# Kernel tuning notes

Measured on AMD Instinct MI355X. Metric: run time of the kernel, lower is better.

## Reference

```python
import jax, jax.numpy as jnp
import numpy as np

N, E, EL = 100000, 1600000, 200000
DIN, DH, DOUT = 128, 128, 64


def _glorot(k, fi, fo):
    return jax.random.normal(k, (fi, fo), jnp.float32) * jax.lax.rsqrt(jnp.float32(fi))


def setup_inputs() -> dict:
    key = jax.random.key(0)
    ks = jax.random.split(key, 8)
    x = jax.random.normal(ks[0], (N, DIN), jnp.float32)
    edge_index = jax.random.randint(ks[1], (2, E), 0, N)
    edge_label_index = jax.random.randint(ks[2], (2, EL), 0, N)
    return {
        "x": x,
        "W1": _glorot(ks[3], DIN, DH), "b1": jnp.zeros((DH,), jnp.float32),
        "W2": _glorot(ks[4], DH, DH), "b2": jnp.zeros((DH,), jnp.float32),
        "W3": _glorot(ks[5], DH, DOUT), "b3": jnp.zeros((DOUT,), jnp.float32),
        "edge_index": edge_index,
        "edge_label_index": edge_label_index,
    }


def gcn_conv(x, W, b, src, dst, norm, n):
    # PyG GCNConv: h = x @ W; out[dst] += norm * h[src]; out += b
    h = x @ W
    msg = h[src] * norm[:, None]                       # [E+N, d]
    out = jax.ops.segment_sum(msg, dst, num_segments=n)
    return out + b


def reference(x, W1, b1, W2, b2, W3, b3, edge_index, edge_label_index):
    n = x.shape[0]
    loop = jnp.arange(n, dtype=edge_index.dtype)
    src = jnp.concatenate([edge_index[0], loop])       # self-loops appended
    dst = jnp.concatenate([edge_index[1], loop])
    # symmetric normalization: deg from dst (col), norm = d^-1/2[src] * d^-1/2[dst]
    deg = jax.ops.segment_sum(jnp.ones(dst.shape[0], x.dtype), dst, num_segments=n)
    dis = jnp.where(deg > 0, jax.lax.rsqrt(jnp.maximum(deg, 1.0)), 0.0)
    norm = dis[src] * dis[dst]

    z = jax.nn.relu(gcn_conv(x, W1, b1, src, dst, norm, n))
    z = jax.nn.relu(gcn_conv(z, W2, b2, src, dst, norm, n))
    z = gcn_conv(z, W3, b3, src, dst, norm, n)

    # decode
    hidden = z[edge_label_index[0]] * z[edge_label_index[1]]   # [EL, DOUT]
    logits = hidden.sum(axis=-1)                               # [EL]
    nrm = jnp.maximum(jnp.linalg.norm(hidden, axis=1, keepdims=True), 1e-12)
    hidden_n = hidden / nrm                                    # F.normalize(dim=1)
    return (hidden_n, logits)
```

## Files before the change

kernel.cpp:

```cpp
#include <hip/hip_runtime.h>
#include <hip/hip_bf16.h>

#define DIN 128
#define DH  128
#define DOUT 64

#define BSHIFT 9
#define BNODES 512
#define BCAP   12288
#define CHUNK  2048

typedef __attribute__((ext_vector_type(8))) short short8;
typedef __attribute__((ext_vector_type(4))) float f32x4;

static __device__ __forceinline__ unsigned short f2bf(float f) {
    unsigned int u = __float_as_uint(f);
    u += 0x7FFFu + ((u >> 16) & 1u);
    return (unsigned short)(u >> 16);
}
static __device__ __forceinline__ float bflo(unsigned int p) {
    return __uint_as_float(p << 16);
}
static __device__ __forceinline__ float bfhi(unsigned int p) {
    return __uint_as_float(p & 0xFFFF0000u);
}

__global__ __launch_bounds__(256) void prep_w_kernel(const float* __restrict__ W1,
                                                     const float* __restrict__ W2,
                                                     const float* __restrict__ W3,
                                                     unsigned short* __restrict__ Wt1,
                                                     unsigned short* __restrict__ Wt2,
                                                     unsigned short* __restrict__ Wt3,
                                                     int* __restrict__ gcur) {
    int i = blockIdx.x * 256 + threadIdx.x;
    if (blockIdx.x == 0) gcur[threadIdx.x] = 0;
    if (i < 128 * 128) {
        int n = i >> 7, k = i & 127;
        Wt1[n * 128 + k] = f2bf(W1[k * 128 + n]);
        Wt2[n * 128 + k] = f2bf(W2[k * 128 + n]);
        if (n < 64) Wt3[n * 128 + k] = f2bf(W3[k * 64 + n]);
    }
}

__global__ __launch_bounds__(256) void bin_scatter_kernel(const int* __restrict__ ei, int E,
                                                          int* __restrict__ gcur,
                                                          int* __restrict__ pairs) {
    __shared__ int hist[256];
    __shared__ int base[256];
    int t = threadIdx.x;
    hist[t] = 0;
    __syncthreads();
    int e0 = blockIdx.x * CHUNK;
    int srcs[8], dsts[8], rk[8];
    #pragma unroll
    for (int j = 0; j < 8; j++) {
        int e = e0 + j * 256 + t;
        if (e < E) {
            srcs[j] = ei[e];
            dsts[j] = ei[E + e];
            rk[j] = atomicAdd(&hist[dsts[j] >> BSHIFT], 1);
        } else {
            rk[j] = -1;
        }
    }
    __syncthreads();
    base[t] = (hist[t] > 0) ? atomicAdd(&gcur[t], hist[t]) : 0;
    __syncthreads();
    #pragma unroll
    for (int j = 0; j < 8; j++) {
        if (rk[j] >= 0) {
            int b = dsts[j] >> BSHIFT;
            int dl = dsts[j] & (BNODES - 1);
            pairs[(size_t)b * BCAP + base[b] + rk[j]] = (dl << 17) | srcs[j];
        }
    }
}

__global__ __launch_bounds__(256) void scan_buckets_kernel(const int* __restrict__ gcur,
                                                           int* __restrict__ bucket_base,
                                                           int nbuck, int n) {
    __shared__ int s[256];
    int t = threadIdx.x;
    int own = 0;
    if (t < nbuck) {
        int lo = t << BSHIFT;
        int cnt = n - lo;
        if (cnt > BNODES) cnt = BNODES;
        if (cnt < 0) cnt = 0;
        own = gcur[t] + cnt;
    }
    s[t] = own;
    __syncthreads();
    for (int off = 1; off < 256; off <<= 1) {
        int v = (t >= off) ? s[t - off] : 0;
        __syncthreads();
        s[t] += v;
        __syncthreads();
    }
    if (t < nbuck) bucket_base[t] = s[t] - own;
}

__global__ __launch_bounds__(1024) void bucket_build_kernel(const int* __restrict__ pairs,
                                                            const int* __restrict__ gcur,
                                                            const int* __restrict__ bucket_base,
                                                            int* __restrict__ row_start,
                                                            float* __restrict__ dis,
                                                            int* __restrict__ csr_src, int n) {
    __shared__ int cnt[BNODES];
    __shared__ int snode[BNODES];
    int t = threadIdx.x, b = blockIdx.x;
    if (t < BNODES) cnt[t] = 0;
    __syncthreads();
    int m = gcur[b];
    const int* p = pairs + (size_t)b * BCAP;
    for (int i = t; i < m; i += 1024) {
        atomicAdd(&cnt[p[i] >> 17], 1);
    }
    __syncthreads();
    if (t < BNODES) {
        int node = (b << BSHIFT) + t;
        snode[t] = (node < n) ? cnt[t] + 1 : 0;
    }
    __syncthreads();
    for (int off = 1; off < BNODES; off <<= 1) {
        int v = (t < BNODES && t >= off) ? snode[t - off] : 0;
        __syncthreads();
        if (t < BNODES) snode[t] += v;
        __syncthreads();
    }
    int bbase = bucket_base[b];
    if (t < BNODES) {
        int node = (b << BSHIFT) + t;
        if (node < n) {
            int deg = cnt[t] + 1;
            int ex = bbase + snode[t] - deg;
            row_start[node] = ex;
            dis[node] = rsqrtf((float)deg);
            csr_src[ex] = node;
            cnt[t] = ex + 1;
            if (node == n - 1) row_start[n] = ex + deg;
        }
    }
    __syncthreads();
    for (int i = t; i < m; i += 1024) {
        int pk = p[i];
        int pos = atomicAdd(&cnt[pk >> 17], 1);
        csr_src[pos] = pk & 0x1FFFF;
    }
}

template <int NOUT, bool AFP32>
__global__ __launch_bounds__(256) void gemm_bf16_kernel(const void* __restrict__ Av,
                                                        const unsigned short* __restrict__ Wt,
                                                        const float* __restrict__ dis,
                                                        unsigned short* __restrict__ H, int M) {
    int wave = (blockIdx.x * 256 + threadIdx.x) >> 6;
    int lane = threadIdx.x & 63;
    int m0 = wave << 4;
    if (m0 >= M) return;
    int m = lane & 15, q = lane >> 4;
    constexpr int NT = NOUT / 16;
    f32x4 acc[NT];
    #pragma unroll
    for (int t = 0; t < NT; t++) acc[t] = (f32x4){0.f, 0.f, 0.f, 0.f};
    const short8* Arow = (const short8*)((const unsigned short*)Av + (size_t)(m0 + m) * 128);
    const float*  Arow32 = (const float*)Av + (size_t)(m0 + m) * 128;
    #pragma unroll
    for (int kk = 0; kk < 4; kk++) {
        short8 a;
        if (AFP32) {
            float4 u = *(const float4*)(Arow32 + kk * 32 + q * 8);
            float4 v = *(const float4*)(Arow32 + kk * 32 + q * 8 + 4);
            a[0] = (short)f2bf(u.x); a[1] = (short)f2bf(u.y);
            a[2] = (short)f2bf(u.z); a[3] = (short)f2bf(u.w);
            a[4] = (short)f2bf(v.x); a[5] = (short)f2bf(v.y);
            a[6] = (short)f2bf(v.z); a[7] = (short)f2bf(v.w);
        } else {
            a = Arow[kk * 4 + q];
        }
        #pragma unroll
        for (int t = 0; t < NT; t++) {
            const short8* Bp = (const short8*)(Wt + (size_t)(t * 16 + m) * 128);
            short8 b = Bp[kk * 4 + q];
            acc[t] = __builtin_amdgcn_mfma_f32_16x16x32_bf16(a, b, acc[t], 0, 0, 0);
        }
    }
    float ds[4];
    #pragma unroll
    for (int r = 0; r < 4; r++) ds[r] = dis[m0 + q * 4 + r];
    #pragma unroll
    for (int t = 0; t < NT; t++)
        #pragma unroll
        for (int r = 0; r < 4; r++)
            H[(size_t)(m0 + q * 4 + r) * NOUT + t * 16 + m] = f2bf(acc[t][r] * ds[r]);
}

template <int NOUT>
__global__ __launch_bounds__(256) void agg_gemm_kernel(const unsigned short* __restrict__ H,
                                                       const int* __restrict__ row_start,
                                                       const int* __restrict__ csr_src,
                                                       const float* __restrict__ dis,
                                                       const float* __restrict__ bias,
                                                       const unsigned short* __restrict__ Wt,
                                                       unsigned short* __restrict__ Hout,
                                                       int n) {
    __shared__ unsigned short X[16][128];
    int t = threadIdx.x;
    int g = t >> 4, gl = t & 15;
    int row = blockIdx.x * 16 + g;
    int c = gl * 8;
    float acc[8];
    #pragma unroll
    for (int i = 0; i < 8; i++) acc[i] = 0.f;
    if (row < n) {
        int p0 = row_start[row], p1 = row_start[row + 1];
        int p = p0;
        for (; p + 8 <= p1; p += 8) {
            int e[8];
            #pragma unroll
            for (int u = 0; u < 8; u++) e[u] = csr_src[p + u];
            uint4 h[8];
            #pragma unroll
            for (int u = 0; u < 8; u++) h[u] = *(const uint4*)(H + (size_t)e[u] * 128 + c);
            #pragma unroll
            for (int u = 0; u < 8; u++) {
                acc[0] += bflo(h[u].x); acc[1] += bfhi(h[u].x);
                acc[2] += bflo(h[u].y); acc[3] += bfhi(h[u].y);
                acc[4] += bflo(h[u].z); acc[5] += bfhi(h[u].z);
                acc[6] += bflo(h[u].w); acc[7] += bfhi(h[u].w);
            }
        }
        for (; p + 4 <= p1; p += 4) {
            int e0 = csr_src[p],     e1 = csr_src[p + 1];
            int e2 = csr_src[p + 2], e3 = csr_src[p + 3];
            uint4 h0 = *(const uint4*)(H + (size_t)e0 * 128 + c);
            uint4 h1 = *(const uint4*)(H + (size_t)e1 * 128 + c);
            uint4 h2 = *(const uint4*)(H + (size_t)e2 * 128 + c);
            uint4 h3 = *(const uint4*)(H + (size_t)e3 * 128 + c);
            acc[0] += bflo(h0.x) + bflo(h1.x) + bflo(h2.x) + bflo(h3.x);
            acc[1] += bfhi(h0.x) + bfhi(h1.x) + bfhi(h2.x) + bfhi(h3.x);
            acc[2] += bflo(h0.y) + bflo(h1.y) + bflo(h2.y) + bflo(h3.y);
            acc[3] += bfhi(h0.y) + bfhi(h1.y) + bfhi(h2.y) + bfhi(h3.y);
            acc[4] += bflo(h0.z) + bflo(h1.z) + bflo(h2.z) + bflo(h3.z);
            acc[5] += bfhi(h0.z) + bfhi(h1.z) + bfhi(h2.z) + bfhi(h3.z);
            acc[6] += bflo(h0.w) + bflo(h1.w) + bflo(h2.w) + bflo(h3.w);
            acc[7] += bfhi(h0.w) + bfhi(h1.w) + bfhi(h2.w) + bfhi(h3.w);
        }
        for (; p < p1; p++) {
            int e = csr_src[p];
            uint4 h = *(const uint4*)(H + (size_t)e * 128 + c);
            acc[0] += bflo(h.x); acc[1] += bfhi(h.x);
            acc[2] += bflo(h.y); acc[3] += bfhi(h.y);
            acc[4] += bflo(h.z); acc[5] += bfhi(h.z);
            acc[6] += bflo(h.w); acc[7] += bfhi(h.w);
        }
        float dd = dis[row];
        #pragma unroll
        for (int i = 0; i < 8; i++)
            acc[i] = fmaxf(acc[i] * dd + bias[c + i], 0.f);
    }
    int wv = t >> 6, lane = t & 63;
    int m = lane & 15, q = lane >> 4;
    constexpr int TPW = NOUT / 64;
    short8 bfrag[4][TPW];
    #pragma unroll
    for (int kk = 0; kk < 4; kk++)
        #pragma unroll
        for (int tt = 0; tt < TPW; tt++) {
            const short8* Bp = (const short8*)(Wt + (size_t)((wv * TPW + tt) * 16 + m) * 128);
            bfrag[kk][tt] = Bp[kk * 4 + q];
        }
    int obase = blockIdx.x * 16;
    float dsout[4];
    #pragma unroll
    for (int r = 0; r < 4; r++) {
        int rr = obase + q * 4 + r;
        dsout[r] = (rr < n) ? dis[rr] : 0.f;
    }
    uint4 pk;
    pk.x = ((unsigned int)f2bf(acc[1]) << 16) | f2bf(acc[0]);
    pk.y = ((unsigned int)f2bf(acc[3]) << 16) | f2bf(acc[2]);
    pk.z = ((unsigned int)f2bf(acc[5]) << 16) | f2bf(acc[4]);
    pk.w = ((unsigned int)f2bf(acc[7]) << 16) | f2bf(acc[6]);
    *(uint4*)&X[g][c ^ ((g & 7) << 3)] = pk;
    __syncthreads();
    f32x4 gacc[TPW];
    #pragma unroll
    for (int tt = 0; tt < TPW; tt++) gacc[tt] = (f32x4){0.f, 0.f, 0.f, 0.f};
    #pragma unroll
    for (int kk = 0; kk < 4; kk++) {
        short8 a = *(const short8*)&X[m][(kk * 32 + q * 8) ^ ((m & 7) << 3)];
        #pragma unroll
        for (int tt = 0; tt < TPW; tt++)
            gacc[tt] = __builtin_amdgcn_mfma_f32_16x16x32_bf16(a, bfrag[kk][tt], gacc[tt], 0, 0, 0);
    }
    #pragma unroll
    for (int r = 0; r < 4; r++) {
        int rr = obase + q * 4 + r;
        if (rr < n) {
            #pragma unroll
            for (int tt = 0; tt < TPW; tt++)
                Hout[(size_t)rr * NOUT + (wv * TPW + tt) * 16 + m] = f2bf(gacc[tt][r] * dsout[r]);
        }
    }
}

template <int EPL, bool RELU, bool OUTBF>
__global__ __launch_bounds__(256) void aggregate_kernel(const unsigned short* __restrict__ H,
                                                        const int* __restrict__ row_start,
                                                        const int* __restrict__ csr_src,
                                                        const float* __restrict__ dis,
                                                        const float* __restrict__ bias,
                                                        void* __restrict__ out, int n) {
    constexpr int F = EPL * 16;
    int row = (blockIdx.x * 256 + threadIdx.x) >> 4;
    int gl  = threadIdx.x & 15;
    if (row >= n) return;
    int c = gl * EPL;
    float acc[EPL];
    #pragma unroll
    for (int i = 0; i < EPL; i++) acc[i] = 0.f;
    int p0 = row_start[row], p1 = row_start[row + 1];
    int p = p0;
    for (; p + 8 <= p1; p += 8) {
        int e[8];
        #pragma unroll
        for (int u = 0; u < 8; u++) e[u] = csr_src[p + u];
        if (EPL == 8) {
            uint4 h[8];
            #pragma unroll
            for (int u = 0; u < 8; u++) h[u] = *(const uint4*)(H + (size_t)e[u] * F + c);
            #pragma unroll
            for (int u = 0; u < 8; u++) {
                acc[0] += bflo(h[u].x); acc[1] += bfhi(h[u].x);
                acc[2] += bflo(h[u].y); acc[3] += bfhi(h[u].y);
                acc[4] += bflo(h[u].z); acc[5] += bfhi(h[u].z);
                acc[6] += bflo(h[u].w); acc[7] += bfhi(h[u].w);
            }
        } else {
            uint2 h[8];
            #pragma unroll
            for (int u = 0; u < 8; u++) h[u] = *(const uint2*)(H + (size_t)e[u] * F + c);
            #pragma unroll
            for (int u = 0; u < 8; u++) {
                acc[0] += bflo(h[u].x); acc[1] += bfhi(h[u].x);
                acc[2] += bflo(h[u].y); acc[3] += bfhi(h[u].y);
            }
        }
    }
    for (; p + 4 <= p1; p += 4) {
        int e0 = csr_src[p],     e1 = csr_src[p + 1];
        int e2 = csr_src[p + 2], e3 = csr_src[p + 3];
        if (EPL == 8) {
            uint4 h0 = *(const uint4*)(H + (size_t)e0 * F + c);
            uint4 h1 = *(const uint4*)(H + (size_t)e1 * F + c);
            uint4 h2 = *(const uint4*)(H + (size_t)e2 * F + c);
            uint4 h3 = *(const uint4*)(H + (size_t)e3 * F + c);
            acc[0] += bflo(h0.x) + bflo(h1.x) + bflo(h2.x) + bflo(h3.x);
            acc[1] += bfhi(h0.x) + bfhi(h1.x) + bfhi(h2.x) + bfhi(h3.x);
            acc[2] += bflo(h0.y) + bflo(h1.y) + bflo(h2.y) + bflo(h3.y);
            acc[3] += bfhi(h0.y) + bfhi(h1.y) + bfhi(h2.y) + bfhi(h3.y);
            acc[4] += bflo(h0.z) + bflo(h1.z) + bflo(h2.z) + bflo(h3.z);
            acc[5] += bfhi(h0.z) + bfhi(h1.z) + bfhi(h2.z) + bfhi(h3.z);
            acc[6] += bflo(h0.w) + bflo(h1.w) + bflo(h2.w) + bflo(h3.w);
            acc[7] += bfhi(h0.w) + bfhi(h1.w) + bfhi(h2.w) + bfhi(h3.w);
        } else {
            uint2 h0 = *(const uint2*)(H + (size_t)e0 * F + c);
            uint2 h1 = *(const uint2*)(H + (size_t)e1 * F + c);
            uint2 h2 = *(const uint2*)(H + (size_t)e2 * F + c);
            uint2 h3 = *(const uint2*)(H + (size_t)e3 * F + c);
            acc[0] += bflo(h0.x) + bflo(h1.x) + bflo(h2.x) + bflo(h3.x);
            acc[1] += bfhi(h0.x) + bfhi(h1.x) + bfhi(h2.x) + bfhi(h3.x);
            acc[2] += bflo(h0.y) + bflo(h1.y) + bflo(h2.y) + bflo(h3.y);
            acc[3] += bfhi(h0.y) + bfhi(h1.y) + bfhi(h2.y) + bfhi(h3.y);
        }
    }
    for (; p < p1; p++) {
        int e = csr_src[p];
        if (EPL == 8) {
            uint4 h = *(const uint4*)(H + (size_t)e * F + c);
            acc[0] += bflo(h.x); acc[1] += bfhi(h.x);
            acc[2] += bflo(h.y); acc[3] += bfhi(h.y);
            acc[4] += bflo(h.z); acc[5] += bfhi(h.z);
            acc[6] += bflo(h.w); acc[7] += bfhi(h.w);
        } else {
            uint2 h = *(const uint2*)(H + (size_t)e * F + c);
            acc[0] += bflo(h.x); acc[1] += bfhi(h.x);
            acc[2] += bflo(h.y); acc[3] += bfhi(h.y);
        }
    }
    float dd = dis[row];
    #pragma unroll
    for (int i = 0; i < EPL; i++) {
        acc[i] = acc[i] * dd + bias[c + i];
        if (RELU) acc[i] = fmaxf(acc[i], 0.f);
    }
    if (OUTBF) {
        unsigned short* ob = (unsigned short*)out + (size_t)row * F + c;
        if (EPL == 8) {
            uint4 pk;
            pk.x = ((unsigned int)f2bf(acc[1]) << 16) | f2bf(acc[0]);
            pk.y = ((unsigned int)f2bf(acc[3]) << 16) | f2bf(acc[2]);
            pk.z = ((unsigned int)f2bf(acc[5]) << 16) | f2bf(acc[4]);
            pk.w = ((unsigned int)f2bf(acc[7]) << 16) | f2bf(acc[6]);
            *(uint4*)ob = pk;
        } else {
            uint2 pk;
            pk.x = ((unsigned int)f2bf(acc[1]) << 16) | f2bf(acc[0]);
            pk.y = ((unsigned int)f2bf(acc[3]) << 16) | f2bf(acc[2]);
            *(uint2*)ob = pk;
        }
    } else {
        float* of = (float*)out + (size_t)row * F + c;
        #pragma unroll
        for (int i = 0; i < EPL; i += 4) {
            *(float4*)(of + i) = make_float4(acc[i], acc[i + 1], acc[i + 2], acc[i + 3]);
        }
    }
}

__global__ __launch_bounds__(256) void decode_kernel(const float* __restrict__ Z,
                                                     const int* __restrict__ eli, int EL,
                                                     float* __restrict__ out_h,
                                                     float* __restrict__ out_l) {
    int g  = (blockIdx.x * 256 + threadIdx.x) >> 4;
    int gl = threadIdx.x & 15;
    int q0 = g * 2;
    if (q0 >= EL) return;
    int q1 = q0 + 1;
    bool has1 = q1 < EL;
    int a0 = eli[q0], b0 = eli[EL + q0];
    int a1 = has1 ? eli[q1] : a0;
    int b1 = has1 ? eli[EL + q1] : b0;
    float4 za0 = *(const float4*)(Z + (size_t)a0 * 64 + gl * 4);
    float4 zb0 = *(const float4*)(Z + (size_t)b0 * 64 + gl * 4);
    float4 za1 = *(const float4*)(Z + (size_t)a1 * 64 + gl * 4);
    float4 zb1 = *(const float4*)(Z + (size_t)b1 * 64 + gl * 4);

    float h00 = za0.x * zb0.x, h01 = za0.y * zb0.y, h02 = za0.z * zb0.z, h03 = za0.w * zb0.w;
    float h10 = za1.x * zb1.x, h11 = za1.y * zb1.y, h12 = za1.z * zb1.z, h13 = za1.w * zb1.w;
    float s0  = h00 + h01 + h02 + h03;
    float ss0 = h00 * h00 + h01 * h01 + h02 * h02 + h03 * h03;
    float s1  = h10 + h11 + h12 + h13;
    float ss1 = h10 * h10 + h11 * h11 + h12 * h12 + h13 * h13;
    #pragma unroll
    for (int off = 8; off > 0; off >>= 1) {
        s0  += __shfl_xor(s0, off, 64);
        ss0 += __shfl_xor(ss0, off, 64);
        s1  += __shfl_xor(s1, off, 64);
        ss1 += __shfl_xor(ss1, off, 64);
    }
    float inv0 = 1.0f / fmaxf(sqrtf(ss0), 1e-12f);
    *(float4*)(out_h + (size_t)q0 * 64 + gl * 4) =
        make_float4(h00 * inv0, h01 * inv0, h02 * inv0, h03 * inv0);
    if (gl == 0) out_l[q0] = s0;
    if (has1) {
        float inv1 = 1.0f / fmaxf(sqrtf(ss1), 1e-12f);
        *(float4*)(out_h + (size_t)q1 * 64 + gl * 4) =
            make_float4(h10 * inv1, h11 * inv1, h12 * inv1, h13 * inv1);
        if (gl == 0) out_l[q1] = s1;
    }
}

extern "C" void kernel_launch(void* const* d_in, const int* in_sizes, int n_in,
                              void* d_out, int out_size, void* d_ws, size_t ws_size,
                              hipStream_t stream) {
    const float* x  = (const float*)d_in[0];
    const float* W1 = (const float*)d_in[1];
    const float* b1 = (const float*)d_in[2];
    const float* W2 = (const float*)d_in[3];
    const float* b2 = (const float*)d_in[4];
    const float* W3 = (const float*)d_in[5];
    const float* b3 = (const float*)d_in[6];
    const int* edge_index = (const int*)d_in[7];
    const int* eli        = (const int*)d_in[8];

    const int N  = in_sizes[0] / DIN;
    const int E  = in_sizes[7] / 2;
    const int EL = in_sizes[8] / 2;
    const int NBUCK = (N + BNODES - 1) >> BSHIFT;

    char* w = (char*)d_ws;
    auto alloc = [&](size_t bytes) -> char* {
        char* p = w; w += (bytes + 255) & ~(size_t)255; return p;
    };
    unsigned short* bufA  = (unsigned short*)alloc((size_t)N * DH * 2);
    unsigned short* bufB  = (unsigned short*)alloc((size_t)N * DH * 2);
    float*          Z3    = (float*)alloc((size_t)N * DOUT * 4);
    unsigned short* Wt1   = (unsigned short*)alloc(128 * 128 * 2);
    unsigned short* Wt2   = (unsigned short*)alloc(128 * 128 * 2);
    unsigned short* Wt3   = (unsigned short*)alloc(64 * 128 * 2);
    int*            row_start = (int*)alloc((size_t)(N + 1) * 4);
    float*          dis    = (float*)alloc((size_t)N * 4);
    int*            gcur   = (int*)alloc(256 * 4);
    int*            bucket_base = (int*)alloc(256 * 4);
    int*            csr_src = (int*)alloc((size_t)(E + N) * 4);
    int*            pairs  = (int*)alloc((size_t)NBUCK * BCAP * 4);

    float* out_h = (float*)d_out;
    float* out_l = out_h + (size_t)EL * DOUT;

    prep_w_kernel<<<64, 256, 0, stream>>>(W1, W2, W3, Wt1, Wt2, Wt3, gcur);
    bin_scatter_kernel<<<(E + CHUNK - 1) / CHUNK, 256, 0, stream>>>(edge_index, E, gcur, pairs);
    scan_buckets_kernel<<<1, 256, 0, stream>>>(gcur, bucket_base, NBUCK, N);
    bucket_build_kernel<<<NBUCK, 1024, 0, stream>>>(pairs, gcur, bucket_base,
                                                    row_start, dis, csr_src, N);

    const int gemm_grid = ((N / 16) * 64 + 255) / 256;
    const int fuse_grid = (N + 15) / 16;
    const int agg_grid  = (N * 16 + 255) / 256;

    gemm_bf16_kernel<128, true><<<gemm_grid, 256, 0, stream>>>(x, Wt1, dis, bufA, N);
    agg_gemm_kernel<128><<<fuse_grid, 256, 0, stream>>>(bufA, row_start, csr_src, dis, b1, Wt2, bufB, N);
    agg_gemm_kernel<64><<<fuse_grid, 256, 0, stream>>>(bufB, row_start, csr_src, dis, b2, Wt3, bufA, N);
    aggregate_kernel<4, false, false><<<agg_grid, 256, 0, stream>>>(bufA, row_start, csr_src, dis, b3, Z3, N);
    const int dec_groups = (EL + 1) / 2;
    decode_kernel<<<(dec_groups * 16 + 255) / 256, 256, 0, stream>>>(Z3, eli, EL, out_h, out_l);
}
```

Before: 390.9 us.

## Process nodes in degree-sorted order to balance aggregation work per wave

Builds a per-bucket degree histogram during CSR construction, scans it, and fills a permutation that groups nodes by in-degree while keeping bucket locality. The aggregation and fused aggregate-GEMM kernels then process rows through this permutation, so the 16-thread groups inside a wave see similar neighbor counts and diverge less. The cost is two extra small kernels plus an indirection, and output rows are written scattered rather than contiguously, which may hurt store coalescing and cache locality.

```diff
diff --git a/kernel.cpp b/kernel.cpp
--- a/kernel.cpp
+++ b/kernel.cpp
@@ -9,6 +9,7 @@
 #define BNODES 512
 #define BCAP   12288
 #define CHUNK  2048
+#define DBINS  64
 
 typedef __attribute__((ext_vector_type(8))) short short8;
 typedef __attribute__((ext_vector_type(4))) float f32x4;
@@ -31,9 +32,11 @@
                                                      unsigned short* __restrict__ Wt1,
                                                      unsigned short* __restrict__ Wt2,
                                                      unsigned short* __restrict__ Wt3,
-                                                     int* __restrict__ gcur) {
+                                                     int* __restrict__ gcur,
+                                                     int* __restrict__ dhist) {
     int i = blockIdx.x * 256 + threadIdx.x;
     if (blockIdx.x == 0) gcur[threadIdx.x] = 0;
+    dhist[i] = 0;
     if (i < 128 * 128) {
         int n = i >> 7, k = i & 127;
         Wt1[n * 128 + k] = f2bf(W1[k * 128 + n]);
@@ -105,11 +108,15 @@
                                                             const int* __restrict__ bucket_base,
                                                             int* __restrict__ row_start,
                                                             float* __restrict__ dis,
-                                                            int* __restrict__ csr_src, int n) {
+                                                            int* __restrict__ csr_src,
+                                                            int* __restrict__ deg_out,
+                                                            int* __restrict__ dhist, int n) {
     __shared__ int cnt[BNODES];
     __shared__ int snode[BNODES];
+    __shared__ int lh[DBINS];
     int t = threadIdx.x, b = blockIdx.x;
     if (t < BNODES) cnt[t] = 0;
+    if (t < DBINS) lh[t] = 0;
     __syncthreads();
     int m = gcur[b];
     const int* p = pairs + (size_t)b * BCAP;
@@ -138,14 +145,54 @@
             dis[node] = rsqrtf((float)deg);
             csr_src[ex] = node;
             cnt[t] = ex + 1;
+            deg_out[node] = deg;
+            int dbin = deg - 1; if (dbin > DBINS - 1) dbin = DBINS - 1;
+            atomicAdd(&lh[dbin], 1);
             if (node == n - 1) row_start[n] = ex + deg;
         }
     }
     __syncthreads();
+    if (t < DBINS && lh[t] > 0) atomicAdd(&dhist[t * 256 + b], lh[t]);
     for (int i = t; i < m; i += 1024) {
         int pk = p[i];
         int pos = atomicAdd(&cnt[pk >> 17], 1);
         csr_src[pos] = pk & 0x1FFFF;
+    }
+}
+
+__global__ __launch_bounds__(1024) void scan_dhist_kernel(int* __restrict__ dhist) {
+    __shared__ int s[1024];
+    int t = threadIdx.x;
+    int v[16];
+    int base = t * 16;
+    int sum = 0;
+    #pragma unroll
+    for (int j = 0; j < 16; j++) { v[j] = dhist[base + j]; sum += v[j]; }
+    s[t] = sum;
+    __syncthreads();
+    for (int off = 1; off < 1024; off <<= 1) {
+        int x = (t >= off) ? s[t - off] : 0;
+        __syncthreads();
+        s[t] += x;
+        __syncthreads();
+    }
+    int run = (t > 0) ? s[t - 1] : 0;
+    #pragma unroll
+    for (int j = 0; j < 16; j++) { int tmp = v[j]; dhist[base + j] = run; run += tmp; }
+}
+
+__global__ __launch_bounds__(512) void perm_fill_kernel(const int* __restrict__ deg,
+                                                        const int* __restrict__ dhist,
+                                                        int* __restrict__ perm, int n) {
+    __shared__ int cur[DBINS];
+    int t = threadIdx.x, b = blockIdx.x;
+    if (t < DBINS) cur[t] = dhist[t * 256 + b];
+    __syncthreads();
+    int node = (b << BSHIFT) + t;
+    if (node < n) {
+        int d = deg[node] - 1; if (d > DBINS - 1) d = DBINS - 1;
+        int pos = atomicAdd(&cur[d], 1);
+        perm[pos] = node;
     }
 }
 
@@ -202,17 +249,19 @@
                                                        const float* __restrict__ dis,
                                                        const float* __restrict__ bias,
                                                        const unsigned short* __restrict__ Wt,
+                                                       const int* __restrict__ perm,
                                                        unsigned short* __restrict__ Hout,
                                                        int n) {
     __shared__ unsigned short X[16][128];
     int t = threadIdx.x;
     int g = t >> 4, gl = t & 15;
-    int row = blockIdx.x * 16 + g;
+    int idx = blockIdx.x * 16 + g;
     int c = gl * 8;
     float acc[8];
     #pragma unroll
     for (int i = 0; i < 8; i++) acc[i] = 0.f;
-    if (row < n) {
+    if (idx < n) {
+        int row = perm[idx];
         int p0 = row_start[row], p1 = row_start[row + 1];
         int p = p0;
         for (; p + 8 <= p1; p += 8) {
@@ -272,10 +321,12 @@
         }
     int obase = blockIdx.x * 16;
     float dsout[4];
+    int rout[4];
     #pragma unroll
     for (int r = 0; r < 4; r++) {
-        int rr = obase + q * 4 + r;
-        dsout[r] = (rr < n) ? dis[rr] : 0.f;
+        int oidx = obase + q * 4 + r;
+        rout[r] = (oidx < n) ? perm[oidx] : -1;
+        dsout[r] = (rout[r] >= 0) ? dis[rout[r]] : 0.f;
     }
     uint4 pk;
     pk.x = ((unsigned int)f2bf(acc[1]) << 16) | f2bf(acc[0]);
@@ -296,11 +347,10 @@
     }
     #pragma unroll
     for (int r = 0; r < 4; r++) {
-        int rr = obase + q * 4 + r;
-        if (rr < n) {
+        if (rout[r] >= 0) {
             #pragma unroll
             for (int tt = 0; tt < TPW; tt++)
-                Hout[(size_t)rr * NOUT + (wv * TPW + tt) * 16 + m] = f2bf(gacc[tt][r] * dsout[r]);
+                Hout[(size_t)rout[r] * NOUT + (wv * TPW + tt) * 16 + m] = f2bf(gacc[tt][r] * dsout[r]);
         }
     }
 }
@@ -311,11 +361,13 @@
                                                         const int* __restrict__ csr_src,
                                                         const float* __restrict__ dis,
                                                         const float* __restrict__ bias,
+                                                        const int* __restrict__ perm,
                                                         void* __restrict__ out, int n) {
     constexpr int F = EPL * 16;
-    int row = (blockIdx.x * 256 + threadIdx.x) >> 4;
+    int idx = (blockIdx.x * 256 + threadIdx.x) >> 4;
     int gl  = threadIdx.x & 15;
-    if (row >= n) return;
+    if (idx >= n) return;
+    int row = perm[idx];
     int c = gl * EPL;
     float acc[EPL];
     #pragma unroll
@@ -492,28 +544,33 @@
     unsigned short* Wt3   = (unsigned short*)alloc(64 * 128 * 2);
     int*            row_start = (int*)alloc((size_t)(N + 1) * 4);
     float*          dis    = (float*)alloc((size_t)N * 4);
+    int*            deg    = (int*)alloc((size_t)N * 4);
+    int*            perm   = (int*)alloc((size_t)N * 4);
     int*            gcur   = (int*)alloc(256 * 4);
     int*            bucket_base = (int*)alloc(256 * 4);
+    int*            dhist  = (int*)alloc(DBINS * 256 * 4);
     int*            csr_src = (int*)alloc((size_t)(E + N) * 4);
     int*            pairs  = (int*)alloc((size_t)NBUCK * BCAP * 4);
 
     float* out_h = (float*)d_out;
     float* out_l = out_h + (size_t)EL * DOUT;
 
-    prep_w_kernel<<<64, 256, 0, stream>>>(W1, W2, W3, Wt1, Wt2, Wt3, gcur);
+    prep_w_kernel<<<64, 256, 0, stream>>>(W1, W2, W3, Wt1, Wt2, Wt3, gcur, dhist);
     bin_scatter_kernel<<<(E + CHUNK - 1) / CHUNK, 256, 0, stream>>>(edge_index, E, gcur, pairs);
     scan_buckets_kernel<<<1, 256, 0, stream>>>(gcur, bucket_base, NBUCK, N);
     bucket_build_kernel<<<NBUCK, 1024, 0, stream>>>(pairs, gcur, bucket_base,
-                                                    row_start, dis, csr_src, N);
+                                                    row_start, dis, csr_src, deg, dhist, N);
+    scan_dhist_kernel<<<1, 1024, 0, stream>>>(dhist);
+    perm_fill_kernel<<<NBUCK, 512, 0, stream>>>(deg, dhist, perm, N);
 
     const int gemm_grid = ((N / 16) * 64 + 255) / 256;
     const int fuse_grid = (N + 15) / 16;
     const int agg_grid  = (N * 16 + 255) / 256;
 
     gemm_bf16_kernel<128, true><<<gemm_grid, 256, 0, stream>>>(x, Wt1, dis, bufA, N);
-    agg_gemm_kernel<128><<<fuse_grid, 256, 0, stream>>>(bufA, row_start, csr_src, dis, b1, Wt2, bufB, N);
-    agg_gemm_kernel<64><<<fuse_grid, 256, 0, stream>>>(bufB, row_start, csr_src, dis, b2, Wt3, bufA, N);
-    aggregate_kernel<4, false, false><<<agg_grid, 256, 0, stream>>>(bufA, row_start, csr_src, dis, b3, Z3, N);
+    agg_gemm_kernel<128><<<fuse_grid, 256, 0, stream>>>(bufA, row_start, csr_src, dis, b1, Wt2, perm, bufB, N);
+    agg_gemm_kernel<64><<<fuse_grid, 256, 0, stream>>>(bufB, row_start, csr_src, dis, b2, Wt3, perm, bufA, N);
+    aggregate_kernel<4, false, false><<<agg_grid, 256, 0, stream>>>(bufA, row_start, csr_src, dis, b3, perm, Z3, N);
     const int dec_groups = (EL + 1) / 2;
     decode_kernel<<<(dec_groups * 16 + 255) / 256, 256, 0, stream>>>(Z3, eli, EL, out_h, out_l);
 }
```

Result: slower. 407.3 us (+4.2%).

## Store features in column-sliced layout and aggregate per 16-feature slice

Applied to the files above, without the earlier changes.

Switches the intermediate node feature buffers to a sliced layout, [slice][node][16] in bf16. Aggregation is split across blocks per slice, so each gather touches a 32-byte slab per neighbour and a slice's working set (about 3.2 MB) can stay cache-resident. The fused aggregate+GEMM kernels are unfused into separate gather and GEMM launches, and the GEMM reads and writes the sliced layout. In exchange, csr_src is re-read once per slice and there are extra launches plus a full intermediate round-trip through memory.

```diff
diff --git a/kernel.cpp b/kernel.cpp
--- a/kernel.cpp
+++ b/kernel.cpp
@@ -163,8 +163,8 @@
     f32x4 acc[NT];
     #pragma unroll
     for (int t = 0; t < NT; t++) acc[t] = (f32x4){0.f, 0.f, 0.f, 0.f};
-    const short8* Arow = (const short8*)((const unsigned short*)Av + (size_t)(m0 + m) * 128);
-    const float*  Arow32 = (const float*)Av + (size_t)(m0 + m) * 128;
+    const float* Arow32 = (const float*)Av + (size_t)(m0 + m) * 128;
+    const unsigned short* Xs = (const unsigned short*)Av;
     #pragma unroll
     for (int kk = 0; kk < 4; kk++) {
         short8 a;
@@ -176,7 +176,8 @@
             a[4] = (short)f2bf(v.x); a[5] = (short)f2bf(v.y);
             a[6] = (short)f2bf(v.z); a[7] = (short)f2bf(v.w);
         } else {
-            a = Arow[kk * 4 + q];
+            int sl = 2 * kk + (q >> 1);
+            a = *(const short8*)(Xs + ((size_t)sl * M + (m0 + m)) * 16 + (q & 1) * 8);
         }
         #pragma unroll
         for (int t = 0; t < NT; t++) {
@@ -192,230 +193,79 @@
     for (int t = 0; t < NT; t++)
         #pragma unroll
         for (int r = 0; r < 4; r++)
-            H[(size_t)(m0 + q * 4 + r) * NOUT + t * 16 + m] = f2bf(acc[t][r] * ds[r]);
-}
-
-template <int NOUT>
-__global__ __launch_bounds__(256) void agg_gemm_kernel(const unsigned short* __restrict__ H,
-                                                       const int* __restrict__ row_start,
-                                                       const int* __restrict__ csr_src,
-                                                       const float* __restrict__ dis,
-                                                       const float* __restrict__ bias,
-                                                       const unsigned short* __restrict__ Wt,
-                                                       unsigned short* __restrict__ Hout,
-                                                       int n) {
-    __shared__ unsigned short X[16][128];
-    int t = threadIdx.x;
-    int g = t >> 4, gl = t & 15;
-    int row = blockIdx.x * 16 + g;
-    int c = gl * 8;
-    float acc[8];
-    #pragma unroll
-    for (int i = 0; i < 8; i++) acc[i] = 0.f;
-    if (row < n) {
-        int p0 = row_start[row], p1 = row_start[row + 1];
-        int p = p0;
-        for (; p + 8 <= p1; p += 8) {
-            int e[8];
-            #pragma unroll
-            for (int u = 0; u < 8; u++) e[u] = csr_src[p + u];
-            uint4 h[8];
-            #pragma unroll
-            for (int u = 0; u < 8; u++) h[u] = *(const uint4*)(H + (size_t)e[u] * 128 + c);
-            #pragma unroll
-            for (int u = 0; u < 8; u++) {
-                acc[0] += bflo(h[u].x); acc[1] += bfhi(h[u].x);
-                acc[2] += bflo(h[u].y); acc[3] += bfhi(h[u].y);
-                acc[4] += bflo(h[u].z); acc[5] += bfhi(h[u].z);
-                acc[6] += bflo(h[u].w); acc[7] += bfhi(h[u].w);
-            }
-        }
-        for (; p + 4 <= p1; p += 4) {
-            int e0 = csr_src[p],     e1 = csr_src[p + 1];
-            int e2 = csr_src[p + 2], e3 = csr_src[p + 3];
-            uint4 h0 = *(const uint4*)(H + (size_t)e0 * 128 + c);
-            uint4 h1 = *(const uint4*)(H + (size_t)e1 * 128 + c);
-            uint4 h2 = *(const uint4*)(H + (size_t)e2 * 128 + c);
-            uint4 h3 = *(const uint4*)(H + (size_t)e3 * 128 + c);
-            acc[0] += bflo(h0.x) + bflo(h1.x) + bflo(h2.x) + bflo(h3.x);
-            acc[1] += bfhi(h0.x) + bfhi(h1.x) + bfhi(h2.x) + bfhi(h3.x);
-            acc[2] += bflo(h0.y) + bflo(h1.y) + bflo(h2.y) + bflo(h3.y);
-            acc[3] += bfhi(h0.y) + bfhi(h1.y) + bfhi(h2.y) + bfhi(h3.y);
-            acc[4] += bflo(h0.z) + bflo(h1.z) + bflo(h2.z) + bflo(h3.z);
-            acc[5] += bfhi(h0.z) + bfhi(h1.z) + bfhi(h2.z) + bfhi(h3.z);
-            acc[6] += bflo(h0.w) + bflo(h1.w) + bflo(h2.w) + bflo(h3.w);
-            acc[7] += bfhi(h0.w) + bfhi(h1.w) + bfhi(h2.w) + bfhi(h3.w);
-        }
-        for (; p < p1; p++) {
-            int e = csr_src[p];
-            uint4 h = *(const uint4*)(H + (size_t)e * 128 + c);
-            acc[0] += bflo(h.x); acc[1] += bfhi(h.x);
-            acc[2] += bflo(h.y); acc[3] += bfhi(h.y);
-            acc[4] += bflo(h.z); acc[5] += bfhi(h.z);
-            acc[6] += bflo(h.w); acc[7] += bfhi(h.w);
-        }
-        float dd = dis[row];
-        #pragma unroll
-        for (int i = 0; i < 8; i++)
-            acc[i] = fmaxf(acc[i] * dd + bias[c + i], 0.f);
-    }
-    int wv = t >> 6, lane = t & 63;
-    int m = lane & 15, q = lane >> 4;
-    constexpr int TPW = NOUT / 64;
-    short8 bfrag[4][TPW];
-    #pragma unroll
-    for (int kk = 0; kk < 4; kk++)
-        #pragma unroll
-        for (int tt = 0; tt < TPW; tt++) {
-            const short8* Bp = (const short8*)(Wt + (size_t)((wv * TPW + tt) * 16 + m) * 128);
-            bfrag[kk][tt] = Bp[kk * 4 + q];
-        }
-    int obase = blockIdx.x * 16;
-    float dsout[4];
-    #pragma unroll
-    for (int r = 0; r < 4; r++) {
-        int rr = obase + q * 4 + r;
-        dsout[r] = (rr < n) ? dis[rr] : 0.f;
-    }
-    uint4 pk;
-    pk.x = ((unsigned int)f2bf(acc[1]) << 16) | f2bf(acc[0]);
-    pk.y = ((unsigned int)f2bf(acc[3]) << 16) | f2bf(acc[2]);
-    pk.z = ((unsigned int)f2bf(acc[5]) << 16) | f2bf(acc[4]);
-    pk.w = ((unsigned int)f2bf(acc[7]) << 16) | f2bf(acc[6]);
-    *(uint4*)&X[g][c ^ ((g & 7) << 3)] = pk;
-    __syncthreads();
-    f32x4 gacc[TPW];
-    #pragma unroll
-    for (int tt = 0; tt < TPW; tt++) gacc[tt] = (f32x4){0.f, 0.f, 0.f, 0.f};
-    #pragma unroll
-    for (int kk = 0; kk < 4; kk++) {
-        short8 a = *(const short8*)&X[m][(kk * 32 + q * 8) ^ ((m & 7) << 3)];
-        #pragma unroll
-        for (int tt = 0; tt < TPW; tt++)
-            gacc[tt] = __builtin_amdgcn_mfma_f32_16x16x32_bf16(a, bfrag[kk][tt], gacc[tt], 0, 0, 0);
-    }
-    #pragma unroll
-    for (int r = 0; r < 4; r++) {
-        int rr = obase + q * 4 + r;
-        if (rr < n) {
-            #pragma unroll
-            for (int tt = 0; tt < TPW; tt++)
-                Hout[(size_t)rr * NOUT + (wv * TPW + tt) * 16 + m] = f2bf(gacc[tt][r] * dsout[r]);
-        }
-    }
-}
-
-template <int EPL, bool RELU, bool OUTBF>
-__global__ __launch_bounds__(256) void aggregate_kernel(const unsigned short* __restrict__ H,
+            H[((size_t)t * M + (m0 + q * 4 + r)) * 16 + m] = f2bf(acc[t][r] * ds[r]);
+}
+
+template <int NSLICE, bool RELU, bool OUTBF>
+__global__ __launch_bounds__(256) void agg_slice_kernel(const unsigned short* __restrict__ H,
                                                         const int* __restrict__ row_start,
                                                         const int* __restrict__ csr_src,
                                                         const float* __restrict__ dis,
                                                         const float* __restrict__ bias,
                                                         void* __restrict__ out, int n) {
-    constexpr int F = EPL * 16;
-    int row = (blockIdx.x * 256 + threadIdx.x) >> 4;
-    int gl  = threadIdx.x & 15;
+    int s = blockIdx.x % NSLICE;
+    int chunk = blockIdx.x / NSLICE;
+    int t = threadIdx.x;
+    int row = chunk * 64 + (t >> 2);
+    int l = t & 3;
     if (row >= n) return;
-    int c = gl * EPL;
-    float acc[EPL];
-    #pragma unroll
-    for (int i = 0; i < EPL; i++) acc[i] = 0.f;
+    const unsigned short* Hs = H + (size_t)s * n * 16;
+    int c = l * 4;
+    float a0 = 0.f, a1 = 0.f, a2 = 0.f, a3 = 0.f;
     int p0 = row_start[row], p1 = row_start[row + 1];
     int p = p0;
     for (; p + 8 <= p1; p += 8) {
         int e[8];
         #pragma unroll
-        for (int u = 0; u < 8; u++) e[u] = csr_src[p + u];
-        if (EPL == 8) {
-            uint4 h[8];
-            #pragma unroll
-            for (int u = 0; u < 8; u++) h[u] = *(const uint4*)(H + (size_t)e[u] * F + c);
-            #pragma unroll
-            for (int u = 0; u < 8; u++) {
-                acc[0] += bflo(h[u].x); acc[1] += bfhi(h[u].x);
-                acc[2] += bflo(h[u].y); acc[3] += bfhi(h[u].y);
-                acc[4] += bflo(h[u].z); acc[5] += bfhi(h[u].z);
-                acc[6] += bflo(h[u].w); acc[7] += bfhi(h[u].w);
-            }
-        } else {
-            uint2 h[8];
-            #pragma unroll
-            for (int u = 0; u < 8; u++) h[u] = *(const uint2*)(H + (size_t)e[u] * F + c);
-            #pragma unroll
-            for (int u = 0; u < 8; u++) {
-                acc[0] += bflo(h[u].x); acc[1] += bfhi(h[u].x);
-                acc[2] += bflo(h[u].y); acc[3] += bfhi(h[u].y);
-            }
+        for (int u = 0; u < 8; u++) e[u] = __builtin_nontemporal_load(&csr_src[p + u]);
+        uint2 h[8];
+        #pragma unroll
+        for (int u = 0; u < 8; u++) h[u] = *(const uint2*)(Hs + (size_t)e[u] * 16 + c);
+        #pragma unroll
+        for (int u = 0; u < 8; u++) {
+            a0 += bflo(h[u].x); a1 += bfhi(h[u].x);
+            a2 += bflo(h[u].y); a3 += bfhi(h[u].y);
         }
     }
     for (; p + 4 <= p1; p += 4) {
-        int e0 = csr_src[p],     e1 = csr_src[p + 1];
-        int e2 = csr_src[p + 2], e3 = csr_src[p + 3];
-        if (EPL == 8) {
-            uint4 h0 = *(const uint4*)(H + (size_t)e0 * F + c);
-            uint4 h1 = *(const uint4*)(H + (size_t)e1 * F + c);
-            uint4 h2 = *(const uint4*)(H + (size_t)e2 * F + c);
-            uint4 h3 = *(const uint4*)(H + (size_t)e3 * F + c);
-            acc[0] += bflo(h0.x) + bflo(h1.x) + bflo(h2.x) + bflo(h3.x);
-            acc[1] += bfhi(h0.x) + bfhi(h1.x) + bfhi(h2.x) + bfhi(h3.x);
-            acc[2] += bflo(h0.y) + bflo(h1.y) + bflo(h2.y) + bflo(h3.y);
-            acc[3] += bfhi(h0.y) + bfhi(h1.y) + bfhi(h2.y) + bfhi(h3.y);
-            acc[4] += bflo(h0.z) + bflo(h1.z) + bflo(h2.z) + bflo(h3.z);
-            acc[5] += bfhi(h0.z) + bfhi(h1.z) + bfhi(h2.z) + bfhi(h3.z);
-            acc[6] += bflo(h0.w) + bflo(h1.w) + bflo(h2.w) + bflo(h3.w);
-            acc[7] += bfhi(h0.w) + bfhi(h1.w) + bfhi(h2.w) + bfhi(h3.w);
-        } else {
-            uint2 h0 = *(const uint2*)(H + (size_t)e0 * F + c);
-            uint2 h1 = *(const uint2*)(H + (size_t)e1 * F + c);
-            uint2 h2 = *(const uint2*)(H + (size_t)e2 * F + c);
-            uint2 h3 = *(const uint2*)(H + (size_t)e3 * F + c);
-            acc[0] += bflo(h0.x) + bflo(h1.x) + bflo(h2.x) + bflo(h3.x);
-            acc[1] += bfhi(h0.x) + bfhi(h1.x) + bfhi(h2.x) + bfhi(h3.x);
-            acc[2] += bflo(h0.y) + bflo(h1.y) + bflo(h2.y) + bflo(h3.y);
-            acc[3] += bfhi(h0.y) + bfhi(h1.y) + bfhi(h2.y) + bfhi(h3.y);
-        }
+        int e0 = __builtin_nontemporal_load(&csr_src[p]);
+        int e1 = __builtin_nontemporal_load(&csr_src[p + 1]);
+        int e2 = __builtin_nontemporal_load(&csr_src[p + 2]);
+        int e3 = __builtin_nontemporal_load(&csr_src[p + 3]);
+        uint2 h0 = *(const uint2*)(Hs + (size_t)e0 * 16 + c);
+        uint2 h1 = *(const uint2*)(Hs + (size_t)e1 * 16 + c);
+        uint2 h2 = *(const uint2*)(Hs + (size_t)e2 * 16 + c);
+        uint2 h3 = *(const uint2*)(Hs + (size_t)e3 * 16 + c);
+        a0 += bflo(h0.x) + bflo(h1.x) + bflo(h2.x) + bflo(h3.x);
+        a1 += bfhi(h0.x) + bfhi(h1.x) + bfhi(h2.x) + bfhi(h3.x);
+        a2 += bflo(h0.y) + bflo(h1.y) + bflo(h2.y) + bflo(h3.y);
+        a3 += bfhi(h0.y) + bfhi(h1.y) + bfhi(h2.y) + bfhi(h3.y);
     }
     for (; p < p1; p++) {
-        int e = csr_src[p];
-        if (EPL == 8) {
-            uint4 h = *(const uint4*)(H + (size_t)e * F + c);
-            acc[0] += bflo(h.x); acc[1] += bfhi(h.x);
-            acc[2] += bflo(h.y); acc[3] += bfhi(h.y);
-            acc[4] += bflo(h.z); acc[5] += bfhi(h.z);
-            acc[6] += bflo(h.w); acc[7] += bfhi(h.w);
-        } else {
-            uint2 h = *(const uint2*)(H + (size_t)e * F + c);
-            acc[0] += bflo(h.x); acc[1] += bfhi(h.x);
-            acc[2] += bflo(h.y); acc[3] += bfhi(h.y);
-        }
+        int e = __builtin_nontemporal_load(&csr_src[p]);
+        uint2 h = *(const uint2*)(Hs + (size_t)e * 16 + c);
+        a0 += bflo(h.x); a1 += bfhi(h.x);
+        a2 += bflo(h.y); a3 += bfhi(h.y);
     }
     float dd = dis[row];
-    #pragma unroll
-    for (int i = 0; i < EPL; i++) {
-        acc[i] = acc[i] * dd + bias[c + i];
-        if (RELU) acc[i] = fmaxf(acc[i], 0.f);
+    int bc = s * 16 + c;
+    a0 = a0 * dd + bias[bc];
+    a1 = a1 * dd + bias[bc + 1];
+    a2 = a2 * dd + bias[bc + 2];
+    a3 = a3 * dd + bias[bc + 3];
+    if (RELU) {
+        a0 = fmaxf(a0, 0.f); a1 = fmaxf(a1, 0.f);
+        a2 = fmaxf(a2, 0.f); a3 = fmaxf(a3, 0.f);
     }
     if (OUTBF) {
-        unsigned short* ob = (unsigned short*)out + (size_t)row * F + c;
-        if (EPL == 8) {
-            uint4 pk;
-            pk.x = ((unsigned int)f2bf(acc[1]) << 16) | f2bf(acc[0]);
-            pk.y = ((unsigned int)f2bf(acc[3]) << 16) | f2bf(acc[2]);
-            pk.z = ((unsigned int)f2bf(acc[5]) << 16) | f2bf(acc[4]);
-            pk.w = ((unsigned int)f2bf(acc[7]) << 16) | f2bf(acc[6]);
-            *(uint4*)ob = pk;
-        } else {
-            uint2 pk;
-            pk.x = ((unsigned int)f2bf(acc[1]) << 16) | f2bf(acc[0]);
-            pk.y = ((unsigned int)f2bf(acc[3]) << 16) | f2bf(acc[2]);
-            *(uint2*)ob = pk;
-        }
+        unsigned short* ob = (unsigned short*)out + (size_t)s * n * 16 + (size_t)row * 16 + c;
+        uint2 pk;
+        pk.x = ((unsigned int)f2bf(a1) << 16) | f2bf(a0);
+        pk.y = ((unsigned int)f2bf(a3) << 16) | f2bf(a2);
+        *(uint2*)ob = pk;
     } else {
-        float* of = (float*)out + (size_t)row * F + c;
-        #pragma unroll
-        for (int i = 0; i < EPL; i += 4) {
-            *(float4*)(of + i) = make_float4(acc[i], acc[i + 1], acc[i + 2], acc[i + 3]);
-        }
+        float* of = (float*)out + (size_t)row * (NSLICE * 16) + bc;
+        *(float4*)of = make_float4(a0, a1, a2, a3);
     }
 }
 
@@ -507,13 +357,14 @@
                                                     row_start, dis, csr_src, N);
 
     const int gemm_grid = ((N / 16) * 64 + 255) / 256;
-    const int fuse_grid = (N + 15) / 16;
-    const int agg_grid  = (N * 16 + 255) / 256;
+    const int chunks    = (N + 63) / 64;
 
     gemm_bf16_kernel<128, true><<<gemm_grid, 256, 0, stream>>>(x, Wt1, dis, bufA, N);
-    agg_gemm_kernel<128><<<fuse_grid, 256, 0, stream>>>(bufA, row_start, csr_src, dis, b1, Wt2, bufB, N);
-    agg_gemm_kernel<64><<<fuse_grid, 256, 0, stream>>>(bufB, row_start, csr_src, dis, b2, Wt3, bufA, N);
-    aggregate_kernel<4, false, false><<<agg_grid, 256, 0, stream>>>(bufA, row_start, csr_src, dis, b3, Z3, N);
+    agg_slice_kernel<8, true, true><<<chunks * 8, 256, 0, stream>>>(bufA, row_start, csr_src, dis, b1, bufB, N);
+    gemm_bf16_kernel<128, false><<<gemm_grid, 256, 0, stream>>>(bufB, Wt2, dis, bufA, N);
+    agg_slice_kernel<8, true, true><<<chunks * 8, 256, 0, stream>>>(bufA, row_start, csr_src, dis, b2, bufB, N);
+    gemm_bf16_kernel<64, false><<<gemm_grid, 256, 0, stream>>>(bufB, Wt3, dis, bufA, N);
+    agg_slice_kernel<4, false, false><<<chunks * 4, 256, 0, stream>>>(bufA, row_start, csr_src, dis, b3, Z3, N);
     const int dec_groups = (EL + 1) / 2;
     decode_kernel<<<(dec_groups * 16 + 255) / 256, 256, 0, stream>>>(Z3, eli, EL, out_h, out_l);
 }
```

Result: slower. 614.5 us (+57.2%).
